# Kernel tuning notes

Measured on AMD Instinct MI355X. Metric: run time of the kernel, lower is better.

Reference implementation:

```python
import jax, jax.numpy as jnp
import numpy as np

N_NODES = 50000
N_EDGES = 800000
FEAT = 128
OUT = 128
BATCH = 2


def setup_inputs() -> dict:
    key = jax.random.key(0)
    k_h, k_w1, k_w2, k_a, k_src, k_dst = jax.random.split(key, 6)
    h = jax.random.normal(k_h, (BATCH, N_NODES, FEAT), dtype=jnp.float32)
    # xavier-uniform-ish scale for params
    W1 = jax.random.normal(k_w1, (FEAT, FEAT), dtype=jnp.float32) * (1.414 / np.sqrt(FEAT))
    W2 = jax.random.normal(k_w2, (FEAT, OUT), dtype=jnp.float32) * (1.414 / np.sqrt(FEAT))
    a = jax.random.normal(k_a, (2 * FEAT, 1), dtype=jnp.float32) * 0.05
    src = jax.random.randint(k_src, (N_EDGES,), 0, N_NODES, dtype=jnp.int32)
    dst = jax.random.randint(k_dst, (N_EDGES,), 0, N_NODES, dtype=jnp.int32)
    return {"h": h, "W1": W1, "W2": W2, "a": a, "src": src, "dst": dst}


def reference(h, W1, W2, a, src, dst):
    B, N, F = h.shape
    g = jnp.einsum('bnf,fk->bnk', h, W1)                      # [B,N,F]
    # cat([g_i, g_j]) @ a  ==  g_i @ a[:F] + g_j @ a[F:]
    s_i = g @ a[:F, 0]                                        # [B,N]
    s_j = g @ a[F:, 0]                                        # [B,N]
    e = jax.nn.leaky_relu(s_i[:, src] + s_j[:, dst], 0.2)     # [B,E]
    # segment softmax over edges grouped by src node
    eT = e.T                                                  # [E,B]
    m = jax.ops.segment_max(eT, src, num_segments=N)          # [N,B]
    ex = jnp.exp(eT - m[src])                                 # [E,B]
    denom = jax.ops.segment_sum(ex, src, num_segments=N)      # [N,B]
    alpha = (ex / denom[src]).T                               # [B,E]
    msg = g[:, dst] * alpha[..., None]                        # [B,E,F]
    h_prime = jnp.zeros_like(g).at[:, src].add(msg)           # scatter-add onto src
    return jax.nn.relu(jnp.einsum('bnf,fo->bno', h_prime, W2))
```

## Files before the change

### kernel.cpp

```cpp
#include <hip/hip_runtime.h>
#include <hip/hip_bf16.h>
#include <cfloat>

#define N_NODES 50000
#define N_EDGES 800000
#define FEAT 128
#define BATCH 2
#define RTOT (BATCH*N_NODES)

typedef __bf16 bf16x8 __attribute__((ext_vector_type(8)));
typedef float  f32x4  __attribute__((ext_vector_type(4)));

__device__ inline unsigned short f2bf(float f){
  unsigned int u = __float_as_uint(f);
  u = (u + 0x7fffu + ((u >> 16) & 1u)) >> 16;
  return (unsigned short)u;
}

__global__ void k_prep(const float* __restrict__ W1, const float* __restrict__ W2,
                       __bf16* __restrict__ W1t, __bf16* __restrict__ W2t,
                       int* __restrict__ cnt){
  int i = blockIdx.x*blockDim.x + threadIdx.x;
  if(i < FEAT*FEAT){
    int k = i >> 7, col = i & 127;
    int sw = (col << 7) + (k ^ ((col & 7) << 3));
    W1t[sw] = (__bf16)W1[i];
    W2t[sw] = (__bf16)W2[i];
  }
  if(i < N_NODES) cnt[i] = 0;
}

__global__ __launch_bounds__(256) void k_gemm1_mfma(const float* __restrict__ h,
        const __bf16* __restrict__ W1t, const float* __restrict__ a,
        __bf16* __restrict__ g, float* __restrict__ s_i, float* __restrict__ s_j)
{
  __shared__ __bf16 Bs[FEAT*FEAT];
  int t = threadIdx.x, lane = t & 63, wid = t >> 6;
  {
    const float4* srcp = (const float4*)W1t;
    float4* dstp = (float4*)Bs;
    for(int i = t; i < FEAT*FEAT/8; i += 256) dstp[i] = srcp[i];
  }
  __syncthreads();

  int rb = blockIdx.x*64 + wid*16;
  int r  = rb + (lane & 15);
  int kq = (lane >> 4) * 8;

  bf16x8 af[4];
  if(r < RTOT){
    const float* hrow = h + (size_t)r*FEAT + kq;
    #pragma unroll
    for(int ks = 0; ks < 4; ks++){
      float4 p0 = *(const float4*)(hrow + ks*32);
      float4 p1 = *(const float4*)(hrow + ks*32 + 4);
      bf16x8 v;
      v[0]=(__bf16)p0.x; v[1]=(__bf16)p0.y; v[2]=(__bf16)p0.z; v[3]=(__bf16)p0.w;
      v[4]=(__bf16)p1.x; v[5]=(__bf16)p1.y; v[6]=(__bf16)p1.z; v[7]=(__bf16)p1.w;
      af[ks] = v;
    }
  } else {
    #pragma unroll
    for(int ks = 0; ks < 4; ks++){ bf16x8 z = {}; af[ks] = z; }
  }

  f32x4 acc[8] = {};
  #pragma unroll
  for(int cb = 0; cb < 8; cb++){
    int col = cb*16 + (lane & 15);
    int swbase = (col << 7);
    int swx = ((col & 7) << 3);
    #pragma unroll
    for(int ks = 0; ks < 4; ks++){
      int kb = ks*32 + kq;
      bf16x8 bf = *(const bf16x8*)&Bs[swbase + (kb ^ swx)];
      acc[cb] = __builtin_amdgcn_mfma_f32_16x16x32_bf16(af[ks], bf, acc[cb], 0, 0, 0);
    }
  }

  int hgrp = lane >> 4;
  float pi[4] = {0,0,0,0}, pj[4] = {0,0,0,0};
  #pragma unroll
  for(int cb = 0; cb < 8; cb++){
    int col = cb*16 + (lane & 15);
    float al = a[col], ah = a[FEAT + col];
    #pragma unroll
    for(int reg = 0; reg < 4; reg++){
      int row = rb + hgrp*4 + reg;
      float v = acc[cb][reg];
      if(row < RTOT){
        int b = (row >= N_NODES) ? 1 : 0;
        int n = row - b*N_NODES;
        g[(size_t)n*256 + b*128 + col] = (__bf16)v;
      }
      pi[reg] = fmaf(v, al, pi[reg]);
      pj[reg] = fmaf(v, ah, pj[reg]);
    }
  }
  #pragma unroll
  for(int reg = 0; reg < 4; reg++){
    #pragma unroll
    for(int m = 1; m < 16; m <<= 1){
      pi[reg] += __shfl_xor(pi[reg], m, 64);
      pj[reg] += __shfl_xor(pj[reg], m, 64);
    }
  }
  if((lane & 15) == 0){
    #pragma unroll
    for(int reg = 0; reg < 4; reg++){
      int row = rb + hgrp*4 + reg;
      if(row < RTOT){
        int b = (row >= N_NODES) ? 1 : 0;
        int n = row - b*N_NODES;
        s_i[n*2 + b] = pi[reg];
        s_j[n*2 + b] = pj[reg];
      }
    }
  }
}

__global__ void k_hist(const int* __restrict__ src, int* __restrict__ cnt){
  int e = blockIdx.x*blockDim.x+threadIdx.x;
  if(e<N_EDGES) atomicAdd(&cnt[src[e]], 1);
}
__global__ __launch_bounds__(1024) void k_scan_a(const int* __restrict__ cnt, int* __restrict__ bsum){
  __shared__ int s[1024];
  int t=threadIdx.x; int idx = blockIdx.x*1024+t;
  s[t] = (idx<N_NODES)? cnt[idx] : 0;
  __syncthreads();
  for(int st=512; st>0; st>>=1){ if(t<st) s[t]+=s[t+st]; __syncthreads(); }
  if(t==0) bsum[blockIdx.x]=s[0];
}
__global__ void k_scan_b(int* __restrict__ bsum, int nb){
  int t=threadIdx.x;
  int v0 = (t<nb)? bsum[t] : 0;
  int v = v0;
  for(int st=1; st<64; st<<=1){
    int u = __shfl_up(v, st, 64);
    if(t>=st) v += u;
  }
  if(t<nb) bsum[t] = v - v0;
}
__global__ __launch_bounds__(1024) void k_scan_c(const int* __restrict__ cnt, const int* __restrict__ bsum,
                                                 int* __restrict__ off, int* __restrict__ curs){
  __shared__ int s[1024];
  int t=threadIdx.x; int idx=blockIdx.x*1024+t;
  int v=(idx<N_NODES)? cnt[idx]:0;
  s[t]=v; __syncthreads();
  for(int st=1; st<1024; st<<=1){
    int u = (t>=st)? s[t-st] : 0;
    __syncthreads();
    s[t] += u;
    __syncthreads();
  }
  if(idx<N_NODES){ int o = bsum[blockIdx.x] + s[t] - v; off[idx]=o; curs[idx]=o; }
}
__global__ void k_fill(const int* __restrict__ src, const int* __restrict__ dst,
                       int* __restrict__ curs, int* __restrict__ dste){
  int e=blockIdx.x*blockDim.x+threadIdx.x;
  if(e<N_EDGES){ int pos = atomicAdd(&curs[src[e]],1); dste[pos]=dst[e]; }
}

__global__ __launch_bounds__(256) void k_agg(const unsigned int* __restrict__ g,
     const float* __restrict__ s_i, const float* __restrict__ s_j,
     const int* __restrict__ cnt, const int* __restrict__ off,
     const int* __restrict__ dste, unsigned int* __restrict__ hp)
{
  int widb = threadIdx.x>>6, lane = threadIdx.x&63;
  int n = blockIdx.x*4 + widb;
  if(n >= N_NODES) return;
  int deg = cnt[n], o0 = off[n];
  int half = lane >> 5, li = lane & 31;
  float si = s_i[n*2 + half];
  int selp = lane & 32;

  float m = -FLT_MAX, denom = 0.f;
  float a0=0.f, a1=0.f, a2=0.f, a3=0.f;

  for(int base=0; base<deg; base+=32){
    int i = base + li;
    int d = 0; float x = -FLT_MAX;
    if(i < deg){
      d = dste[o0 + i];
      float xx = si + s_j[d*2 + half];
      x = (xx > 0.f) ? xx : 0.2f*xx;
    }
    float cm = x;
    #pragma unroll
    for(int mm=16; mm; mm>>=1) cm = fmaxf(cm, __shfl_xor(cm, mm, 64));
    float mn = fmaxf(m, cm);
    float scale = __expf(m - mn);
    float p = (i < deg) ? __expf(x - mn) : 0.f;
    denom = denom*scale + p;
    a0*=scale; a1*=scale; a2*=scale; a3*=scale;
    m = mn;

    int lim = min(32, deg-base);
    int lim8 = (lim + 7) & ~7;
    for(int j=0; j<lim8; j+=8){
      float q[8]; int e[8];
      #pragma unroll
      for(int c=0;c<8;c++){
        q[c] = __shfl(p, selp | (j+c), 64);
        e[c] = __shfl(d, j+c, 64);
      }
      uint2 u[8];
      #pragma unroll
      for(int c=0;c<8;c++) u[c] = *(const uint2*)(g + (size_t)e[c]*128 + lane*2);
      #pragma unroll
      for(int c=0;c<8;c++){
        a0 = fmaf(q[c], __uint_as_float(u[c].x << 16),         a0);
        a1 = fmaf(q[c], __uint_as_float(u[c].x & 0xffff0000u), a1);
        a2 = fmaf(q[c], __uint_as_float(u[c].y << 16),         a2);
        a3 = fmaf(q[c], __uint_as_float(u[c].y & 0xffff0000u), a3);
      }
    }
  }
  #pragma unroll
  for(int mm=16; mm; mm>>=1) denom += __shfl_xor(denom, mm, 64);
  float inv = (denom > 0.f) ? 1.0f/denom : 0.f;
  unsigned int w0 = ((unsigned int)f2bf(a1*inv) << 16) | f2bf(a0*inv);
  unsigned int w1 = ((unsigned int)f2bf(a3*inv) << 16) | f2bf(a2*inv);
  uint2 o; o.x = w0; o.y = w1;
  *(uint2*)(hp + (size_t)n*128 + lane*2) = o;
}

__global__ __launch_bounds__(256) void k_gemm2_mfma(const __bf16* __restrict__ hp,
        const __bf16* __restrict__ W2t, float* __restrict__ out)
{
  __shared__ __bf16 Bs[FEAT*FEAT];
  int t = threadIdx.x, lane = t & 63, wid = t >> 6;
  {
    const float4* srcp = (const float4*)W2t;
    float4* dstp = (float4*)Bs;
    for(int i = t; i < FEAT*FEAT/8; i += 256) dstp[i] = srcp[i];
  }
  __syncthreads();

  int rb = blockIdx.x*64 + wid*16;
  int r  = rb + (lane & 15);
  int kq = (lane >> 4) * 8;

  bf16x8 af[4];
  if(r < RTOT){
    const __bf16* hrow = hp + (size_t)r*FEAT + kq;
    #pragma unroll
    for(int ks = 0; ks < 4; ks++) af[ks] = *(const bf16x8*)(hrow + ks*32);
  } else {
    #pragma unroll
    for(int ks = 0; ks < 4; ks++){ bf16x8 z = {}; af[ks] = z; }
  }

  f32x4 acc[8] = {};
  #pragma unroll
  for(int cb = 0; cb < 8; cb++){
    int col = cb*16 + (lane & 15);
    int swbase = (col << 7);
    int swx = ((col & 7) << 3);
    #pragma unroll
    for(int ks = 0; ks < 4; ks++){
      int kb = ks*32 + kq;
      bf16x8 bf = *(const bf16x8*)&Bs[swbase + (kb ^ swx)];
      acc[cb] = __builtin_amdgcn_mfma_f32_16x16x32_bf16(af[ks], bf, acc[cb], 0, 0, 0);
    }
  }

  int hgrp = lane >> 4;
  #pragma unroll
  for(int cb = 0; cb < 8; cb++){
    int col = cb*16 + (lane & 15);
    #pragma unroll
    for(int reg = 0; reg < 4; reg++){
      int ri = rb + hgrp*4 + reg;
      if(ri < RTOT){
        int orow = (ri & 1)*N_NODES + (ri >> 1);
        out[(size_t)orow*FEAT + col] = fmaxf(acc[cb][reg], 0.f);
      }
    }
  }
}

extern "C" void kernel_launch(void* const* d_in, const int* in_sizes, int n_in,
                              void* d_out, int out_size, void* d_ws, size_t ws_size,
                              hipStream_t stream) {
  const float* h  = (const float*)d_in[0];
  const float* W1 = (const float*)d_in[1];
  const float* W2 = (const float*)d_in[2];
  const float* a  = (const float*)d_in[3];
  const int* src  = (const int*)d_in[4];
  const int* dst  = (const int*)d_in[5];
  float* out = (float*)d_out;

  char* w = (char*)d_ws;
  __bf16* g   = (__bf16*)w;                          w += (size_t)RTOT*FEAT*2;
  __bf16* hp  = (__bf16*)w;                          w += (size_t)RTOT*FEAT*2;
  float* s_i  = (float*)w;                           w += (size_t)RTOT*4;
  float* s_j  = (float*)w;                           w += (size_t)RTOT*4;
  __bf16* W1t = (__bf16*)w;                          w += FEAT*FEAT*2;
  __bf16* W2t = (__bf16*)w;                          w += FEAT*FEAT*2;
  int* cnt  = (int*)w;                               w += N_NODES*4;
  int* off  = (int*)w;                               w += N_NODES*4;
  int* curs = (int*)w;                               w += N_NODES*4;
  int* dste = (int*)w;                               w += N_EDGES*4;
  int* bsum = (int*)w;

  k_prep<<<(N_NODES+255)/256,256,0,stream>>>(W1,W2,W1t,W2t,cnt);

  int gemm_grid = (RTOT + 63)/64;
  k_gemm1_mfma<<<gemm_grid,256,0,stream>>>(h,W1t,a,g,s_i,s_j);

  k_hist<<<(N_EDGES+255)/256,256,0,stream>>>(src,cnt);
  int nb=(N_NODES+1023)/1024;
  k_scan_a<<<nb,1024,0,stream>>>(cnt,bsum);
  k_scan_b<<<1,64,0,stream>>>(bsum,nb);
  k_scan_c<<<nb,1024,0,stream>>>(cnt,bsum,off,curs);
  k_fill<<<(N_EDGES+255)/256,256,0,stream>>>(src,dst,curs,dste);

  k_agg<<<(N_NODES+3)/4,256,0,stream>>>((const unsigned int*)g,s_i,s_j,cnt,off,dste,(unsigned int*)hp);

  k_gemm2_mfma<<<gemm_grid,256,0,stream>>>(hp,W2t,out);
}
```

Baseline: 199.3 us.

## Fuse histogram into GEMM1, merge scans, drop max pass in aggregation

Result: faster. 181.7 us (-8.8%).

```diff
diff --git a/kernel.cpp b/kernel.cpp
--- a/kernel.cpp
+++ b/kernel.cpp
@@ -1,5 +1,6 @@
 #include <hip/hip_runtime.h>
 #include <hip/hip_bf16.h>
+#include <hip/hip_fp16.h>
 #include <cfloat>
 
 #define N_NODES 50000
@@ -32,7 +33,8 @@
 
 __global__ __launch_bounds__(256) void k_gemm1_mfma(const float* __restrict__ h,
         const __bf16* __restrict__ W1t, const float* __restrict__ a,
-        __bf16* __restrict__ g, float* __restrict__ s_i, float* __restrict__ s_j)
+        __bf16* __restrict__ g, float* __restrict__ s_i, float* __restrict__ s_j,
+        const int* __restrict__ src, int* __restrict__ cnt)
 {
   __shared__ __bf16 Bs[FEAT*FEAT];
   int t = threadIdx.x, lane = t & 63, wid = t >> 6;
@@ -117,48 +119,52 @@
       }
     }
   }
-}
-
-__global__ void k_hist(const int* __restrict__ src, int* __restrict__ cnt){
-  int e = blockIdx.x*blockDim.x+threadIdx.x;
-  if(e<N_EDGES) atomicAdd(&cnt[src[e]], 1);
-}
-__global__ __launch_bounds__(1024) void k_scan_a(const int* __restrict__ cnt, int* __restrict__ bsum){
+
+  int gs = gridDim.x * 256;
+  for(int e = blockIdx.x*256 + t; e < N_EDGES; e += gs)
+    atomicAdd(&cnt[src[e]], 1);
+}
+
+__global__ __launch_bounds__(1024) void k_scan1(const int* __restrict__ cnt,
+                                                int* __restrict__ off, int* __restrict__ bsum){
   __shared__ int s[1024];
-  int t=threadIdx.x; int idx = blockIdx.x*1024+t;
-  s[t] = (idx<N_NODES)? cnt[idx] : 0;
-  __syncthreads();
-  for(int st=512; st>0; st>>=1){ if(t<st) s[t]+=s[t+st]; __syncthreads(); }
-  if(t==0) bsum[blockIdx.x]=s[0];
-}
-__global__ void k_scan_b(int* __restrict__ bsum, int nb){
-  int t=threadIdx.x;
-  int v0 = (t<nb)? bsum[t] : 0;
-  int v = v0;
-  for(int st=1; st<64; st<<=1){
-    int u = __shfl_up(v, st, 64);
-    if(t>=st) v += u;
-  }
-  if(t<nb) bsum[t] = v - v0;
-}
-__global__ __launch_bounds__(1024) void k_scan_c(const int* __restrict__ cnt, const int* __restrict__ bsum,
-                                                 int* __restrict__ off, int* __restrict__ curs){
-  __shared__ int s[1024];
-  int t=threadIdx.x; int idx=blockIdx.x*1024+t;
-  int v=(idx<N_NODES)? cnt[idx]:0;
-  s[t]=v; __syncthreads();
-  for(int st=1; st<1024; st<<=1){
-    int u = (t>=st)? s[t-st] : 0;
+  int t = threadIdx.x, idx = blockIdx.x*1024 + t;
+  int v = (idx < N_NODES) ? cnt[idx] : 0;
+  s[t] = v; __syncthreads();
+  for(int st = 1; st < 1024; st <<= 1){
+    int u = (t >= st) ? s[t-st] : 0;
     __syncthreads();
     s[t] += u;
     __syncthreads();
   }
-  if(idx<N_NODES){ int o = bsum[blockIdx.x] + s[t] - v; off[idx]=o; curs[idx]=o; }
+  if(idx < N_NODES) off[idx] = s[t] - v;
+  if(t == 1023) bsum[blockIdx.x] = s[t];
+}
+__global__ __launch_bounds__(1024) void k_scan2(int* __restrict__ off,
+                                                const int* __restrict__ bsum, int* __restrict__ curs){
+  __shared__ int pfx;
+  int t = threadIdx.x, idx = blockIdx.x*1024 + t;
+  if(t < 64){
+    int nb = (N_NODES + 1023)/1024;
+    int v0 = (t < nb) ? bsum[t] : 0;
+    int v = v0;
+    for(int st = 1; st < 64; st <<= 1){
+      int u = __shfl_up(v, st, 64);
+      if(t >= st) v += u;
+    }
+    if(t == blockIdx.x) pfx = v - v0;
+  }
+  __syncthreads();
+  if(idx < N_NODES){
+    int o = off[idx] + pfx;
+    off[idx] = o;
+    curs[idx] = o;
+  }
 }
 __global__ void k_fill(const int* __restrict__ src, const int* __restrict__ dst,
                        int* __restrict__ curs, int* __restrict__ dste){
-  int e=blockIdx.x*blockDim.x+threadIdx.x;
-  if(e<N_EDGES){ int pos = atomicAdd(&curs[src[e]],1); dste[pos]=dst[e]; }
+  int e = blockIdx.x*blockDim.x + threadIdx.x;
+  if(e < N_EDGES){ int pos = atomicAdd(&curs[src[e]], 1); dste[pos] = dst[e]; }
 }
 
 __global__ __launch_bounds__(256) void k_agg(const unsigned int* __restrict__ g,
@@ -174,39 +180,32 @@
   float si = s_i[n*2 + half];
   int selp = lane & 32;
 
-  float m = -FLT_MAX, denom = 0.f;
+  float denom = 0.f;
   float a0=0.f, a1=0.f, a2=0.f, a3=0.f;
 
   for(int base=0; base<deg; base+=32){
     int i = base + li;
-    int d = 0; float x = -FLT_MAX;
+    unsigned int w = 0;
     if(i < deg){
-      d = dste[o0 + i];
+      int d = dste[o0 + i];
       float xx = si + s_j[d*2 + half];
-      x = (xx > 0.f) ? xx : 0.2f*xx;
-    }
-    float cm = x;
-    #pragma unroll
-    for(int mm=16; mm; mm>>=1) cm = fmaxf(cm, __shfl_xor(cm, mm, 64));
-    float mn = fmaxf(m, cm);
-    float scale = __expf(m - mn);
-    float p = (i < deg) ? __expf(x - mn) : 0.f;
-    denom = denom*scale + p;
-    a0*=scale; a1*=scale; a2*=scale; a3*=scale;
-    m = mn;
-
+      float x = (xx > 0.f) ? xx : 0.2f*xx;
+      float p = __expf(x);
+      denom += p;
+      w = ((unsigned int)__half_as_ushort(__float2half(p)) << 16) | (unsigned int)d;
+    }
     int lim = min(32, deg-base);
     int lim8 = (lim + 7) & ~7;
     for(int j=0; j<lim8; j+=8){
-      float q[8]; int e[8];
+      unsigned int ww[8];
+      #pragma unroll
+      for(int c=0;c<8;c++) ww[c] = __shfl(w, selp | (j+c), 64);
+      uint2 u[8]; float q[8];
       #pragma unroll
       for(int c=0;c<8;c++){
-        q[c] = __shfl(p, selp | (j+c), 64);
-        e[c] = __shfl(d, j+c, 64);
-      }
-      uint2 u[8];
-      #pragma unroll
-      for(int c=0;c<8;c++) u[c] = *(const uint2*)(g + (size_t)e[c]*128 + lane*2);
+        q[c] = __half2float(__ushort_as_half((unsigned short)(ww[c] >> 16)));
+        u[c] = *(const uint2*)(g + (size_t)(ww[c] & 0xffffu)*128 + lane*2);
+      }
       #pragma unroll
       for(int c=0;c<8;c++){
         a0 = fmaf(q[c], __uint_as_float(u[c].x << 16),         a0);
@@ -307,13 +306,11 @@
   k_prep<<<(N_NODES+255)/256,256,0,stream>>>(W1,W2,W1t,W2t,cnt);
 
   int gemm_grid = (RTOT + 63)/64;
-  k_gemm1_mfma<<<gemm_grid,256,0,stream>>>(h,W1t,a,g,s_i,s_j);
-
-  k_hist<<<(N_EDGES+255)/256,256,0,stream>>>(src,cnt);
-  int nb=(N_NODES+1023)/1024;
-  k_scan_a<<<nb,1024,0,stream>>>(cnt,bsum);
-  k_scan_b<<<1,64,0,stream>>>(bsum,nb);
-  k_scan_c<<<nb,1024,0,stream>>>(cnt,bsum,off,curs);
+  k_gemm1_mfma<<<gemm_grid,256,0,stream>>>(h,W1t,a,g,s_i,s_j,src,cnt);
+
+  int nb = (N_NODES+1023)/1024;
+  k_scan1<<<nb,1024,0,stream>>>(cnt,off,bsum);
+  k_scan2<<<nb,1024,0,stream>>>(off,bsum,curs);
   k_fill<<<(N_EDGES+255)/256,256,0,stream>>>(src,dst,curs,dste);
 
   k_agg<<<(N_NODES+3)/4,256,0,stream>>>((const unsigned int*)g,s_i,s_j,cnt,off,dste,(unsigned int*)hp);
```
